# Kernel tuning notes

Hardware: AMD Instinct MI355X
Metric: run time of the kernel (lower is better)

## Reference

```python
import jax, jax.numpy as jnp
import numpy as np

B, D, G, H = 65536, 512, 16, 128


def setup_inputs() -> dict:
    key = jax.random.key(0)
    ks = jax.random.split(key, 8)
    s = 1.0 / np.sqrt(D)
    sh = 1.0 / np.sqrt(H)
    return {
        "z": jax.random.normal(ks[0], (B, D), dtype=jnp.float32),
        "Wc": jax.random.uniform(ks[1], (D, G), jnp.float32, -s, s),
        "bc": jax.random.uniform(ks[2], (G,), jnp.float32, -s, s),
        "W1": jax.random.uniform(ks[3], (G, D, H), jnp.float32, -s, s),
        "b1": jax.random.uniform(ks[4], (G, H), jnp.float32, -s, s),
        "W2": jax.random.uniform(ks[5], (G, H), jnp.float32, -sh, sh),
        "b2": jax.random.uniform(ks[6], (G,), jnp.float32, -sh, sh),
    }


def reference(z, Wc, bc, W1, b1, W2, b2):
    # classifier head + softmax
    logits = z @ Wc + bc                                  # [B, G]
    p_g = jax.nn.softmax(logits, axis=1)                  # [B, G]
    # G experts fused as one batched GEMM: fc1 -> GELU -> fc2 (dropout = identity at eval)
    h = jax.nn.gelu(jnp.einsum('bd,gdh->bgh', z, W1) + b1, approximate=False)  # [B, G, H]
    y_all = jnp.einsum('bgh,gh->bg', h, W2) + b2          # [B, G]
    return logits, p_g, y_all
```

## Files before the change

kernel.cpp:

```cpp
#include <hip/hip_runtime.h>
#include <cstdint>
#include <cstddef>

typedef __bf16 bf16x8 __attribute__((ext_vector_type(8)));
typedef float f32x4 __attribute__((ext_vector_type(4)));
typedef unsigned short ushortx4 __attribute__((ext_vector_type(4)));

__device__ __forceinline__ unsigned short f2bf(float f) {
  union { float f; unsigned int u; } v; v.f = f;
  return (unsigned short)((v.u + 0x8000u) >> 16);
}

__device__ __forceinline__ float gelu_s(float x) {
  float x2 = x * x;
  float p = __builtin_fmaf(x2, -0.10294324f, -2.30220819f);
  float e = __builtin_amdgcn_exp2f(x * p);
  return x * __builtin_amdgcn_rcpf(1.0f + e);
}

#define GLOAD16(gsrc, ldst)                                                  \
  __builtin_amdgcn_global_load_lds(                                          \
      (const __attribute__((address_space(1))) unsigned int*)(gsrc),         \
      (__attribute__((address_space(3))) unsigned int*)(uintptr_t)(          \
          (char*)(ldst)),                                                    \
      16, 0, 0)

#define SWZ_FRAG(base, R, C8)                                                \
  (*(const bf16x8*)((base) + (((R) >> 5) * 4096) +                           \
                    ((((R)&31) * 8 + ((C8) ^ ((R)&7))) * 16)))

__device__ __forceinline__ void expert_tile(
    int e, int mbase, const unsigned short* __restrict__ zb,
    const unsigned short* __restrict__ w1t, const float* __restrict__ b1,
    const float* __restrict__ w2, const float* __restrict__ b2,
    float* __restrict__ out, char* lds, int tid, int wq, int l15, int l4,
    int c8s) {
  char* ldsB = lds + 16384;
  const unsigned short* ag = zb + (size_t)(mbase + (tid >> 3)) * 512 + c8s;
  const unsigned short* bg = w1t + e * 65536 + (tid >> 3) * 512 + c8s;
  const int wr = wq >> 1;
  const int wc = wq & 1;
  f32x4 acc[4][4] = {};
  for (int kt = 0; kt < 8; ++kt) {
    const int ko = kt * 64;
#pragma unroll
    for (int it = 0; it < 4; ++it)
      GLOAD16(ag + it * 32 * 512 + ko, lds + it * 4096 + tid * 16);
#pragma unroll
    for (int it = 0; it < 4; ++it)
      GLOAD16(bg + it * 32 * 512 + ko, ldsB + it * 4096 + tid * 16);
    __syncthreads();
#pragma unroll
    for (int ks = 0; ks < 2; ++ks) {
      bf16x8 af[4];
#pragma unroll
      for (int rt = 0; rt < 4; ++rt)
        af[rt] = SWZ_FRAG(lds, wr * 64 + rt * 16 + l15, ks * 4 + l4);
#pragma unroll
      for (int ct = 0; ct < 4; ++ct) {
        bf16x8 bfv = SWZ_FRAG(ldsB, wc * 64 + ct * 16 + l15, ks * 4 + l4);
#pragma unroll
        for (int rt = 0; rt < 4; ++rt)
          acc[rt][ct] = __builtin_amdgcn_mfma_f32_16x16x32_bf16(
              af[rt], bfv, acc[rt][ct], 0, 0, 0);
      }
    }
    __syncthreads();
  }
  float b1v[4], w2v[4];
#pragma unroll
  for (int ct = 0; ct < 4; ++ct) {
    int n = wc * 64 + ct * 16 + l15;
    b1v[ct] = b1[e * 128 + n];
    w2v[ct] = w2[e * 128 + n];
  }
  float* ylds = (float*)(lds + 32768);
#pragma unroll
  for (int rt = 0; rt < 4; ++rt) {
#pragma unroll
    for (int i = 0; i < 4; ++i) {
      float s = 0.0f;
#pragma unroll
      for (int ct = 0; ct < 4; ++ct)
        s += gelu_s(acc[rt][ct][i] + b1v[ct]) * w2v[ct];
#pragma unroll
      for (int off = 1; off < 16; off <<= 1) s += __shfl_xor(s, off, 16);
      if (l15 == 0) ylds[wq * 64 + rt * 16 + l4 * 4 + i] = s;
    }
  }
  __syncthreads();
  if (tid < 128) {
    int rl = tid & 63, half = tid >> 6;
    float y = ylds[half * 128 + rl] + ylds[half * 128 + 64 + rl] + b2[e];
    out[(size_t)2097152 + (size_t)(mbase + half * 64 + rl) * 16 + e] = y;
  }
}

__device__ __forceinline__ void logits_tile(
    int mbase, const unsigned short* __restrict__ zb,
    const unsigned short* __restrict__ wct, const float* __restrict__ bc,
    float* __restrict__ out, char* lds, int tid, int wq, int l15, int l4,
    int c8s) {
  const unsigned short* ag = zb + (size_t)(mbase + (tid >> 3)) * 512 + c8s;
  const unsigned short* wb = wct + l15 * 512 + l4 * 8;
  f32x4 acc2[2] = {};
  for (int kt = 0; kt < 8; ++kt) {
    const int ko = kt * 64;
#pragma unroll
    for (int it = 0; it < 4; ++it)
      GLOAD16(ag + it * 32 * 512 + ko, lds + it * 4096 + tid * 16);
    bf16x8 bfr0 = *(const bf16x8*)(wb + ko);
    bf16x8 bfr1 = *(const bf16x8*)(wb + ko + 32);
    __syncthreads();
#pragma unroll
    for (int rt = 0; rt < 2; ++rt) {
      bf16x8 a0 = SWZ_FRAG(lds, wq * 32 + rt * 16 + l15, l4);
      acc2[rt] =
          __builtin_amdgcn_mfma_f32_16x16x32_bf16(a0, bfr0, acc2[rt], 0, 0, 0);
      bf16x8 a1 = SWZ_FRAG(lds, wq * 32 + rt * 16 + l15, 4 + l4);
      acc2[rt] =
          __builtin_amdgcn_mfma_f32_16x16x32_bf16(a1, bfr1, acc2[rt], 0, 0, 0);
    }
    __syncthreads();
  }
  float bcv = bc[l15];
#pragma unroll
  for (int rt = 0; rt < 2; ++rt) {
#pragma unroll
    for (int i = 0; i < 4; ++i) {
      int row = wq * 32 + rt * 16 + l4 * 4 + i;
      float lg = acc2[rt][i] + bcv;
      float mx = lg;
#pragma unroll
      for (int off = 1; off < 16; off <<= 1)
        mx = fmaxf(mx, __shfl_xor(mx, off, 16));
      float ex = __expf(lg - mx);
      float sm = ex;
#pragma unroll
      for (int off = 1; off < 16; off <<= 1) sm += __shfl_xor(sm, off, 16);
      size_t ro = (size_t)(mbase + row) * 16 + l15;
      out[ro] = lg;
      out[1048576 + ro] = ex / sm;
    }
  }
}

__global__ __launch_bounds__(256, 8) void k_convert(
    const float* __restrict__ z, const float* __restrict__ W1,
    const float* __restrict__ Wc, unsigned short* __restrict__ zb,
    unsigned short* __restrict__ w1t, unsigned short* __restrict__ wct) {
  int bid = blockIdx.x;
  int tid = threadIdx.x;
  if (bid < 2048) {
    const f32x4* z4 = (const f32x4*)z;
    size_t base = (size_t)bid * 4096 + tid;
#pragma unroll
    for (int c = 0; c < 4; ++c) {
      f32x4 a[4];
#pragma unroll
      for (int it = 0; it < 4; ++it)
        a[it] = __builtin_nontemporal_load(z4 + base + (c * 4 + it) * 256);
#pragma unroll
      for (int it = 0; it < 4; ++it) {
        ushortx4 r;
        r[0] = f2bf(a[it][0]); r[1] = f2bf(a[it][1]);
        r[2] = f2bf(a[it][2]); r[3] = f2bf(a[it][3]);
        *(ushortx4*)(zb + (base + (c * 4 + it) * 256) * 4) = r;
      }
    }
  } else if (bid < 2048 + 1024) {
    __shared__ float tile[32][33];
    int b = bid - 2048;
    int gg = b >> 6;
    int t = b & 63;
    int d0 = (t >> 2) * 32;
    int h0 = (t & 3) * 32;
    int tx = tid & 31, ty = tid >> 5;
#pragma unroll
    for (int r = 0; r < 4; ++r)
      tile[r * 8 + ty][tx] = W1[(gg << 16) + (d0 + r * 8 + ty) * 128 + h0 + tx];
    __syncthreads();
#pragma unroll
    for (int r = 0; r < 4; ++r)
      w1t[(gg << 16) + (h0 + r * 8 + ty) * 512 + d0 + tx] =
          f2bf(tile[tx][r * 8 + ty]);
  } else {
#pragma unroll
    for (int j = 0; j < 32; ++j) {
      int i = j * 256 + tid;
      wct[(i & 15) * 512 + (i >> 4)] = f2bf(Wc[i]);
    }
  }
}

__global__ __launch_bounds__(256, 4) void k_main(
    const unsigned short* __restrict__ zb,
    const unsigned short* __restrict__ w1t,
    const unsigned short* __restrict__ wct, const float* __restrict__ bc,
    const float* __restrict__ b1, const float* __restrict__ w2,
    const float* __restrict__ b2, float* __restrict__ out) {
  __shared__ alignas(16) char lds[33792];
  const int tid = threadIdx.x;
  const int wq = tid >> 6;
  const int l15 = tid & 15;
  const int l4 = (tid >> 4) & 3;
  const int c8s = (((tid & 7) ^ ((tid >> 3) & 7))) * 8;
  if (blockIdx.x >= 512) {
    const int eb = blockIdx.x - 512;
    const int idx = (eb & 7) * 1024 + (eb >> 3);
    expert_tile(idx & 15, (idx >> 4) * 128, zb, w1t, b1, w2, b2, out, lds, tid,
                wq, l15, l4, c8s);
  } else {
    logits_tile(blockIdx.x * 128, zb, wct, bc, out, lds, tid, wq, l15, l4,
                c8s);
  }
}

extern "C" void kernel_launch(void* const* d_in, const int* in_sizes, int n_in,
                              void* d_out, int out_size, void* d_ws,
                              size_t ws_size, hipStream_t stream) {
  const float* z = (const float*)d_in[0];
  const float* Wc = (const float*)d_in[1];
  const float* bc = (const float*)d_in[2];
  const float* W1 = (const float*)d_in[3];
  const float* b1 = (const float*)d_in[4];
  const float* W2 = (const float*)d_in[5];
  const float* b2 = (const float*)d_in[6];
  float* out = (float*)d_out;

  unsigned short* zb = (unsigned short*)d_ws;
  unsigned short* w1t = zb + (size_t)65536 * 512;
  unsigned short* wct = w1t + (size_t)16 * 128 * 512;

  k_convert<<<2048 + 1024 + 1, 256, 0, stream>>>(z, W1, Wc, zb, w1t, wct);
  k_main<<<512 + 8192, 256, 0, stream>>>(zb, w1t, wct, bc, b1, W2, b2, out);
}
```

Baseline: 367.5 us.

## Fuse z fp32-to-bf16 conversion into GEMM staging and group blocks per row tile

Removes the separate pass that converted z to bf16 in workspace. The main kernel now loads fp32 z directly, converts it in registers, and writes the bf16 values to LDS, replacing the async global_load_lds path for the A operand. Block indices are remapped so the logits tile and all 16 expert tiles for the same 128-row slab are scheduled together on one XCD, so the fp32 z rows are reused from L2. The cost is twice the bytes per A load, synchronous register staging instead of direct-to-LDS copies, and conversion work repeated 17 times per row tile.

```diff
diff --git a/kernel.cpp b/kernel.cpp
--- a/kernel.cpp
+++ b/kernel.cpp
@@ -4,7 +4,7 @@
 
 typedef __bf16 bf16x8 __attribute__((ext_vector_type(8)));
 typedef float f32x4 __attribute__((ext_vector_type(4)));
-typedef unsigned short ushortx4 __attribute__((ext_vector_type(4)));
+typedef unsigned short ushortx8 __attribute__((ext_vector_type(8)));
 
 __device__ __forceinline__ unsigned short f2bf(float f) {
   union { float f; unsigned int u; } v; v.f = f;
@@ -29,14 +29,34 @@
   (*(const bf16x8*)((base) + (((R) >> 5) * 4096) +                           \
                     ((((R)&31) * 8 + ((C8) ^ ((R)&7))) * 16)))
 
+__device__ __forceinline__ void stage_A_f32(const float* __restrict__ ag,
+                                            char* lds, int tid, int ko) {
+  f32x4 a0[4], a1[4];
+#pragma unroll
+  for (int it = 0; it < 4; ++it) {
+    const float* p = ag + it * 32 * 512 + ko;
+    a0[it] = *(const f32x4*)(p);
+    a1[it] = *(const f32x4*)(p + 4);
+  }
+#pragma unroll
+  for (int it = 0; it < 4; ++it) {
+    ushortx8 r;
+    r[0] = f2bf(a0[it][0]); r[1] = f2bf(a0[it][1]);
+    r[2] = f2bf(a0[it][2]); r[3] = f2bf(a0[it][3]);
+    r[4] = f2bf(a1[it][0]); r[5] = f2bf(a1[it][1]);
+    r[6] = f2bf(a1[it][2]); r[7] = f2bf(a1[it][3]);
+    *(ushortx8*)(lds + it * 4096 + tid * 16) = r;
+  }
+}
+
 __device__ __forceinline__ void expert_tile(
-    int e, int mbase, const unsigned short* __restrict__ zb,
+    int e, int mbase, const float* __restrict__ z,
     const unsigned short* __restrict__ w1t, const float* __restrict__ b1,
     const float* __restrict__ w2, const float* __restrict__ b2,
     float* __restrict__ out, char* lds, int tid, int wq, int l15, int l4,
     int c8s) {
   char* ldsB = lds + 16384;
-  const unsigned short* ag = zb + (size_t)(mbase + (tid >> 3)) * 512 + c8s;
+  const float* ag = z + (size_t)(mbase + (tid >> 3)) * 512 + c8s;
   const unsigned short* bg = w1t + e * 65536 + (tid >> 3) * 512 + c8s;
   const int wr = wq >> 1;
   const int wc = wq & 1;
@@ -45,10 +65,8 @@
     const int ko = kt * 64;
 #pragma unroll
     for (int it = 0; it < 4; ++it)
-      GLOAD16(ag + it * 32 * 512 + ko, lds + it * 4096 + tid * 16);
-#pragma unroll
-    for (int it = 0; it < 4; ++it)
       GLOAD16(bg + it * 32 * 512 + ko, ldsB + it * 4096 + tid * 16);
+    stage_A_f32(ag, lds, tid, ko);
     __syncthreads();
 #pragma unroll
     for (int ks = 0; ks < 2; ++ks) {
@@ -97,18 +115,16 @@
 }
 
 __device__ __forceinline__ void logits_tile(
-    int mbase, const unsigned short* __restrict__ zb,
+    int mbase, const float* __restrict__ z,
     const unsigned short* __restrict__ wct, const float* __restrict__ bc,
     float* __restrict__ out, char* lds, int tid, int wq, int l15, int l4,
     int c8s) {
-  const unsigned short* ag = zb + (size_t)(mbase + (tid >> 3)) * 512 + c8s;
+  const float* ag = z + (size_t)(mbase + (tid >> 3)) * 512 + c8s;
   const unsigned short* wb = wct + l15 * 512 + l4 * 8;
   f32x4 acc2[2] = {};
   for (int kt = 0; kt < 8; ++kt) {
     const int ko = kt * 64;
-#pragma unroll
-    for (int it = 0; it < 4; ++it)
-      GLOAD16(ag + it * 32 * 512 + ko, lds + it * 4096 + tid * 16);
+    stage_A_f32(ag, lds, tid, ko);
     bf16x8 bfr0 = *(const bf16x8*)(wb + ko);
     bf16x8 bfr1 = *(const bf16x8*)(wb + ko + 32);
     __syncthreads();
@@ -145,34 +161,15 @@
   }
 }
 
-__global__ __launch_bounds__(256, 8) void k_convert(
-    const float* __restrict__ z, const float* __restrict__ W1,
-    const float* __restrict__ Wc, unsigned short* __restrict__ zb,
+__global__ __launch_bounds__(256) void k_convert(
+    const float* __restrict__ W1, const float* __restrict__ Wc,
     unsigned short* __restrict__ w1t, unsigned short* __restrict__ wct) {
   int bid = blockIdx.x;
   int tid = threadIdx.x;
-  if (bid < 2048) {
-    const f32x4* z4 = (const f32x4*)z;
-    size_t base = (size_t)bid * 4096 + tid;
-#pragma unroll
-    for (int c = 0; c < 4; ++c) {
-      f32x4 a[4];
-#pragma unroll
-      for (int it = 0; it < 4; ++it)
-        a[it] = __builtin_nontemporal_load(z4 + base + (c * 4 + it) * 256);
-#pragma unroll
-      for (int it = 0; it < 4; ++it) {
-        ushortx4 r;
-        r[0] = f2bf(a[it][0]); r[1] = f2bf(a[it][1]);
-        r[2] = f2bf(a[it][2]); r[3] = f2bf(a[it][3]);
-        *(ushortx4*)(zb + (base + (c * 4 + it) * 256) * 4) = r;
-      }
-    }
-  } else if (bid < 2048 + 1024) {
+  if (bid < 1024) {
     __shared__ float tile[32][33];
-    int b = bid - 2048;
-    int gg = b >> 6;
-    int t = b & 63;
+    int gg = bid >> 6;
+    int t = bid & 63;
     int d0 = (t >> 2) * 32;
     int h0 = (t & 3) * 32;
     int tx = tid & 31, ty = tid >> 5;
@@ -194,8 +191,7 @@
 }
 
 __global__ __launch_bounds__(256, 4) void k_main(
-    const unsigned short* __restrict__ zb,
-    const unsigned short* __restrict__ w1t,
+    const float* __restrict__ z, const unsigned short* __restrict__ w1t,
     const unsigned short* __restrict__ wct, const float* __restrict__ bc,
     const float* __restrict__ b1, const float* __restrict__ w2,
     const float* __restrict__ b2, float* __restrict__ out) {
@@ -205,13 +201,15 @@
   const int l15 = tid & 15;
   const int l4 = (tid >> 4) & 3;
   const int c8s = (((tid & 7) ^ ((tid >> 3) & 7))) * 8;
-  if (blockIdx.x >= 512) {
-    const int eb = blockIdx.x - 512;
-    const int idx = (eb & 7) * 1024 + (eb >> 3);
-    expert_tile(idx & 15, (idx >> 4) * 128, zb, w1t, b1, w2, b2, out, lds, tid,
-                wq, l15, l4, c8s);
+  const int xcd = blockIdx.x & 7;
+  const int t = blockIdx.x >> 3;
+  const int pl = t / 17;
+  const int r = t - pl * 17;
+  const int mbase = (xcd * 64 + pl) * 128;
+  if (r == 0) {
+    logits_tile(mbase, z, wct, bc, out, lds, tid, wq, l15, l4, c8s);
   } else {
-    logits_tile(blockIdx.x * 128, zb, wct, bc, out, lds, tid, wq, l15, l4,
+    expert_tile(r - 1, mbase, z, w1t, b1, w2, b2, out, lds, tid, wq, l15, l4,
                 c8s);
   }
 }
@@ -228,10 +226,9 @@
   const float* b2 = (const float*)d_in[6];
   float* out = (float*)d_out;
 
-  unsigned short* zb = (unsigned short*)d_ws;
-  unsigned short* w1t = zb + (size_t)65536 * 512;
+  unsigned short* w1t = (unsigned short*)d_ws;
   unsigned short* wct = w1t + (size_t)16 * 128 * 512;
 
-  k_convert<<<2048 + 1024 + 1, 256, 0, stream>>>(z, W1, Wc, zb, w1t, wct);
-  k_main<<<512 + 8192, 256, 0, stream>>>(zb, w1t, wct, bc, b1, W2, b2, out);
-}
+  k_convert<<<1024 + 1, 256, 0, stream>>>(W1, Wc, w1t, wct);
+  k_main<<<8 * 1088, 256, 0, stream>>>(z, w1t, wct, bc, b1, W2, b2, out);
+}
```

Measured after the change: 353.6 us. -3.8%, faster.
